# Performance work log

Measured on AMD Instinct MI355X. Metric: run time of the kernel, lower is better.

The kernel has to match this reference:

```python
import jax, jax.numpy as jnp
import numpy as np

G, N, D = 512, 400, 128   # graphs, nodes per graph, feature dim
K = 200                   # max_node_num (cluster slots per graph)
DOUT = 512
DMID = DOUT // 16         # 32


def setup_inputs() -> dict:
    key = jax.random.key(0)
    ks = jax.random.split(key, 10)
    x = jax.random.normal(ks[0], (G, N, D), dtype=jnp.float32)
    cluster = jax.random.randint(ks[1], (G, N), 0, K, dtype=jnp.int32)
    true_score = jax.random.uniform(ks[2], (G // 2, 1), dtype=jnp.float32)
    # learned parameters
    W1 = jax.random.normal(ks[3], (D, D), dtype=jnp.float32) / np.sqrt(D)
    b1 = jnp.zeros((D,), jnp.float32)
    W2 = jax.random.normal(ks[4], (DMID, K * D), dtype=jnp.float32) / np.sqrt(K * D)
    b2 = jax.random.normal(ks[5], (DMID,), dtype=jnp.float32) * 0.01
    W3 = jax.random.normal(ks[6], (DOUT, DMID), dtype=jnp.float32) / np.sqrt(DMID)
    b3 = jnp.zeros((DOUT,), jnp.float32)
    return {"x": x, "cluster": cluster, "true_score": true_score,
            "W1": W1, "b1": b1, "W2": W2, "b2": b2, "W3": W3, "b3": b3}


def reference(x, cluster, true_score, W1, b1, W2, b2, W3, b3):
    g, n, d = x.shape
    # avg_pool over clusters (scatter-mean), vectorized across all graphs
    ids = (cluster + jnp.arange(g, dtype=cluster.dtype)[:, None] * K).reshape(-1)
    flat = x.reshape(g * n, d)
    sums = jax.ops.segment_sum(flat, ids, num_segments=g * K)          # [g*K, d]
    cnt = jax.ops.segment_sum(jnp.ones((g * n,), x.dtype), ids, num_segments=g * K)
    pooled = sums / jnp.maximum(cnt, 1.0)[:, None]                     # empty clusters -> 0
    # MLP_1: Linear(D, D) + ReLU, applied per pooled node
    h = jax.nn.relu(pooled @ W1 + b1)                                  # [g*K, d]
    # flatten pooled node set; MLP_2 truncated linear == full weight on zero-padded vec
    h = h.reshape(g, K * d)
    h = jax.nn.relu(h @ W2.T + b2)                                     # [g, 32]
    # MLP_3: Linear(32, 512) + ReLU
    h = jax.nn.relu(h @ W3.T + b3)                                     # [g, 512]
    # cosine similarity between consecutive graph pairs (eps=1e-6 clamp as torch)
    g1, g2 = h[0::2], h[1::2]
    eps = 1e-6
    n1 = jnp.maximum(jnp.sqrt(jnp.sum(g1 * g1, -1)), eps)
    n2 = jnp.maximum(jnp.sqrt(jnp.sum(g2 * g2, -1)), eps)
    scores = (jnp.sum(g1 * g2, -1) / (n1 * n2))[:, None]               # [g//2, 1]
    loss = jnp.mean((scores - true_score) ** 2)                        # MSELoss
    return loss
```

## Files before the change

### kernel.cpp

```cpp
#include <hip/hip_runtime.h>
#include <math.h>

#define G 512
#define N 400
#define D 128
#define K 200
#define DOUT 512
#define DMID 32
#define GK (G*K)
#define KD (K*D)
#define NCHUNK 200

#define SH  129
#define SW2 36

#define KQ 25

__device__ __forceinline__ float relu(float v) { return fmaxf(v, 0.0f); }

typedef __attribute__((ext_vector_type(8))) short short8b;
typedef __attribute__((ext_vector_type(16))) float floatx16;

__device__ __forceinline__ ushort f2bf(float f) {
  unsigned u = __float_as_uint(f);
  unsigned r = (u + 0x7FFFu + ((u >> 16) & 1u)) >> 16;
  return (ushort)r;
}
__device__ __forceinline__ float bf2f(ushort h) {
  return __uint_as_float(((unsigned)h) << 16);
}

__global__ __launch_bounds__(256) void w1prep(
    const float* __restrict__ W1, ushort* __restrict__ wh, ushort* __restrict__ wl) {
  const int idx = blockIdx.x * 256 + threadIdx.x;
  const int i = idx & 7, l = (idx >> 3) & 63, ks = (idx >> 9) & 7, nt = idx >> 12;
  const int k = ks * 16 + (l >> 5) * 8 + i;
  const int n = nt * 32 + (l & 31);
  const float v = W1[k * D + n];
  const ushort h = f2bf(v);
  wh[idx] = h;
  wl[idx] = f2bf(v - bf2f(h));
}

__global__ __launch_bounds__(256) void pool_gemm1_fused(
    const float* __restrict__ x, const int* __restrict__ cluster,
    const ushort* __restrict__ wh, const ushort* __restrict__ wl,
    const float* __restrict__ b1, float* __restrict__ h1) {
  __shared__ int s_ids[N];
  __shared__ int s_cnt[KQ];
  __shared__ int s_off[KQ + 1];
  __shared__ int s_cur[KQ];
  __shared__ int s_sorted[N];
  __shared__ ushort sAhi[8 * 64 * 8];
  __shared__ ushort sAlo[8 * 64 * 8];
  const int g = blockIdx.y;
  const int kb = blockIdx.x * KQ;
  const int tid = threadIdx.x;
  const int* cg = cluster + g * N;

  for (int i = tid; i < N; i += 256) s_ids[i] = cg[i];
  if (tid < KQ) { s_cnt[tid] = 0; s_cur[tid] = 0; }
  {
    short8b z;
#pragma unroll
    for (int e = 0; e < 8; ++e) z[e] = 0;
    for (int i = tid; i < 512; i += 256) {
      *(short8b*)&sAhi[i * 8] = z;
      *(short8b*)&sAlo[i * 8] = z;
    }
  }
  __syncthreads();

  for (int i = tid; i < N; i += 256) {
    const int id = s_ids[i] - kb;
    if ((unsigned)id < (unsigned)KQ) atomicAdd(&s_cnt[id], 1);
  }
  __syncthreads();

  if (tid < 64) {
    const int cv = (tid < KQ) ? s_cnt[tid] : 0;
    int c = cv;
#pragma unroll
    for (int off = 1; off < 32; off <<= 1) {
      const int t = __shfl_up(c, off);
      if (tid >= off) c += t;
    }
    if (tid < KQ) s_off[tid] = c - cv;
    if (tid == KQ - 1) s_off[KQ] = c;
  }
  __syncthreads();

  for (int i = tid; i < N; i += 256) {
    const int id = s_ids[i] - kb;
    if ((unsigned)id < (unsigned)KQ) {
      const int pos = atomicAdd(&s_cur[id], 1);
      s_sorted[s_off[id] + pos] = (id << 9) | i;
    }
  }
  __syncthreads();

  const int wv = tid >> 6, l = tid & 63;
  {
    const int kl0 = (wv * KQ) >> 2;
    const int kl1 = ((wv + 1) * KQ) >> 2;
    const float* xg = x + (size_t)g * N * D + l * 2;
    const int k0 = 2 * l;
    const int ksL = k0 >> 4, kqL = (k0 >> 3) & 1, i0 = k0 & 7;

#define PL_FLUSH(KL, AX, AY, INV)                                          \
    {                                                                      \
      const int blk = ksL * 64 + ((kqL * 32 + (KL)) ^ ksL);                \
      const float fx = (AX) * (INV), fy = (AY) * (INV);                    \
      const ushort hx = f2bf(fx), hy = f2bf(fy);                           \
      ushort2 hv; hv.x = hx; hv.y = hy;                                    \
      ushort2 lv;                                                          \
      lv.x = f2bf(fx - bf2f(hx)); lv.y = f2bf(fy - bf2f(hy));              \
      *(ushort2*)&sAhi[blk * 8 + i0] = hv;                                 \
      *(ushort2*)&sAlo[blk * 8 + i0] = lv;                                 \
    }

    if (kl1 > kl0) {
      const int i0g = s_off[kl0], i1g = s_off[kl1];
      if (i1g > i0g) {
        int prev = -1;
        float ax = 0.0f, ay = 0.0f;
        int pkA[8], pkB[8];
        float2 vA[8], vB[8];

#define PL_LOAD(PK, VV, BASE)                                              \
        {                                                                  \
          _Pragma("unroll")                                                \
          for (int j = 0; j < 8; ++j) {                                    \
            const int mi = ((BASE) + j < i1g) ? (BASE) + j : i1g - 1;      \
            PK[j] = s_sorted[mi];                                          \
          }                                                                \
          _Pragma("unroll")                                                \
          for (int j = 0; j < 8; ++j)                                      \
            VV[j] = *(const float2*)&xg[(size_t)(PK[j] & 511) * D];        \
        }

#define PL_PROC(PK, VV, BASE)                                              \
        {                                                                  \
          _Pragma("unroll")                                                \
          for (int j = 0; j < 8; ++j) {                                    \
            if ((BASE) + j < i1g) {                                        \
              const int id = PK[j] >> 9;                                   \
              if (id != prev) {                                            \
                if (prev >= 0) {                                           \
                  const float inv = 1.0f / (float)s_cnt[prev];             \
                  PL_FLUSH(prev, ax, ay, inv);                             \
                }                                                          \
                ax = VV[j].x; ay = VV[j].y; prev = id;                     \
              } else { ax += VV[j].x; ay += VV[j].y; }                     \
            }                                                              \
          }                                                                \
        }

        int base = i0g;
        PL_LOAD(pkA, vA, base);
        while (base < i1g) {
          if (base + 8 < i1g) PL_LOAD(pkB, vB, base + 8);
          PL_PROC(pkA, vA, base);
          base += 8;
          if (base >= i1g) break;
          if (base + 8 < i1g) PL_LOAD(pkA, vA, base + 8);
          PL_PROC(pkB, vB, base);
          base += 8;
        }
        if (prev >= 0) {
          const float inv = 1.0f / (float)s_cnt[prev];
          PL_FLUSH(prev, ax, ay, inv);
        }
#undef PL_LOAD
#undef PL_PROC
      }
    }
#undef PL_FLUSH
  }
  __syncthreads();

  floatx16 acc0;
#pragma unroll
  for (int e = 0; e < 16; ++e) acc0[e] = 0.0f;

  const ushort* whw = wh + (size_t)(wv * 8) * 64 * 8;
  const ushort* wlw = wl + (size_t)(wv * 8) * 64 * 8;

#pragma unroll 2
  for (int ks = 0; ks < 8; ++ks) {
    const int lx = l ^ ks;
    const short8b bh = *(const short8b*)&whw[(ks * 64 + l) * 8];
    const short8b bl = *(const short8b*)&wlw[(ks * 64 + l) * 8];
    const short8b ah = *(const short8b*)&sAhi[(ks * 64 + lx) * 8];
    const short8b al = *(const short8b*)&sAlo[(ks * 64 + lx) * 8];
    acc0 = __builtin_amdgcn_mfma_f32_32x32x16_bf16(ah, bh, acc0, 0, 0, 0);
    acc0 = __builtin_amdgcn_mfma_f32_32x32x16_bf16(ah, bl, acc0, 0, 0, 0);
    acc0 = __builtin_amdgcn_mfma_f32_32x32x16_bf16(al, bh, acc0, 0, 0, 0);
  }

  const int col = l & 31;
  const int n = wv * 32 + col;
  const float bias = b1[n];
  const int rbase = 4 * (l >> 5);
  float* hrow = h1 + ((size_t)g * K + kb) * D + n;
#pragma unroll
  for (int e = 0; e < 16; ++e) {
    const int row = (e & 3) + 8 * (e >> 2) + rbase;
    if (row < KQ) hrow[(size_t)row * D] = relu(acc0[e] + bias);
  }
}

__global__ __launch_bounds__(256) void gemm2_partial(
    const float* __restrict__ h1, const float* __restrict__ W2,
    float* __restrict__ partials) {
  extern __shared__ float smem[];
  float* sHt = smem;
  float* sWT = smem + 32 * SH;
  const int kc = blockIdx.x;
  const int gb = blockIdx.y;
  const int k0 = kc * 128, g0 = gb * 32;
  const int tid = threadIdx.x;

  for (int i = tid; i < 32 * 128; i += 256) {
    const int r = i >> 7, k = i & 127;
    sHt[r * SH + k] = h1[(size_t)(g0 + r) * KD + k0 + k];
  }
  for (int i = tid; i < 32 * 128; i += 256) {
    const int j = i >> 7, k = i & 127;
    sWT[k * SW2 + j] = W2[(size_t)j * KD + k0 + k];
  }
  __syncthreads();

  const int jt = tid & 7;
  const int gt = tid >> 3;
  float acc[4];
#pragma unroll
  for (int j = 0; j < 4; j++) acc[j] = 0.0f;

  for (int k = 0; k < 128; ++k) {
    const float h = sHt[gt * SH + k];
    const float4 w0 = *(const float4*)&sWT[k * SW2 + jt * 4];
    acc[0] = fmaf(h, w0.x, acc[0]); acc[1] = fmaf(h, w0.y, acc[1]);
    acc[2] = fmaf(h, w0.z, acc[2]); acc[3] = fmaf(h, w0.w, acc[3]);
  }

  float* pp = partials + ((size_t)kc * G + g0 + gt) * DMID + jt * 4;
  *(float4*)&pp[0] = make_float4(acc[0], acc[1], acc[2], acc[3]);
}

__global__ __launch_bounds__(256) void gemm2_reduce(
    const float* __restrict__ partials, const float* __restrict__ b2,
    float* __restrict__ h2) {
  __shared__ float s_red[3][64];
  const int tid = threadIdx.x;
  const int li = tid & 63;
  const int w = tid >> 6;
  const int idx = blockIdx.x * 64 + li;
  float s = 0.0f;
#pragma unroll 5
  for (int c = w * 50; c < w * 50 + 50; ++c)
    s += partials[(size_t)c * (G * DMID) + idx];
  if (w > 0) s_red[w - 1][li] = s;
  __syncthreads();
  if (w == 0) {
    s += s_red[0][li] + s_red[1][li] + s_red[2][li];
    h2[idx] = relu(s + b2[idx & 31]);
  }
}

__global__ __launch_bounds__(256) void head_kernel(
    const float* __restrict__ h2, const float* __restrict__ W3,
    const float* __restrict__ b3, const float* __restrict__ ts,
    float* __restrict__ pair_sq) {
  __shared__ float sA[DMID], sB[DMID];
  __shared__ float rdot[4], rna[4], rnb[4];
  const int p = blockIdx.x;
  const int tid = threadIdx.x;
  if (tid < DMID) sA[tid] = h2[(size_t)(2 * p) * DMID + tid];
  else if (tid < 2 * DMID) sB[tid - DMID] = h2[(size_t)(2 * p + 1) * DMID + (tid - DMID)];
  __syncthreads();

  float dot = 0.0f, na = 0.0f, nb = 0.0f;
#pragma unroll
  for (int rep = 0; rep < 2; ++rep) {
    const int o = rep * 256 + tid;
    const float* w = W3 + (size_t)o * DMID;
    float accA = b3[o], accB = accA;
#pragma unroll
    for (int m = 0; m < DMID; m += 4) {
      const float4 wv = *(const float4*)&w[m];
      accA = fmaf(sA[m], wv.x, accA); accB = fmaf(sB[m], wv.x, accB);
      accA = fmaf(sA[m + 1], wv.y, accA); accB = fmaf(sB[m + 1], wv.y, accB);
      accA = fmaf(sA[m + 2], wv.z, accA); accB = fmaf(sB[m + 2], wv.z, accB);
      accA = fmaf(sA[m + 3], wv.w, accA); accB = fmaf(sB[m + 3], wv.w, accB);
    }
    const float a = relu(accA), b = relu(accB);
    dot = fmaf(a, b, dot); na = fmaf(a, a, na); nb = fmaf(b, b, nb);
  }
#pragma unroll
  for (int off = 32; off >= 1; off >>= 1) {
    dot += __shfl_down(dot, off);
    na  += __shfl_down(na, off);
    nb  += __shfl_down(nb, off);
  }
  const int wave = tid >> 6, lane = tid & 63;
  if (lane == 0) { rdot[wave] = dot; rna[wave] = na; rnb[wave] = nb; }
  __syncthreads();
  if (tid == 0) {
    const float dt = rdot[0] + rdot[1] + rdot[2] + rdot[3];
    const float nA = rna[0] + rna[1] + rna[2] + rna[3];
    const float nB = rnb[0] + rnb[1] + rnb[2] + rnb[3];
    const float n1 = fmaxf(sqrtf(nA), 1e-6f);
    const float n2 = fmaxf(sqrtf(nB), 1e-6f);
    const float sc = dt / (n1 * n2);
    const float e = sc - ts[p];
    pair_sq[p] = e * e;
  }
}

__global__ __launch_bounds__(256) void loss_kernel(
    const float* __restrict__ pair_sq, float* __restrict__ out) {
  __shared__ float red[4];
  const int tid = threadIdx.x;
  float v = pair_sq[tid];
#pragma unroll
  for (int off = 32; off >= 1; off >>= 1) v += __shfl_down(v, off);
  const int wave = tid >> 6, lane = tid & 63;
  if (lane == 0) red[wave] = v;
  __syncthreads();
  if (tid == 0) out[0] = (red[0] + red[1] + red[2] + red[3]) * (1.0f / 256.0f);
}

extern "C" void kernel_launch(void* const* d_in, const int* in_sizes, int n_in,
                              void* d_out, int out_size, void* d_ws, size_t ws_size,
                              hipStream_t stream) {
  const float* x       = (const float*)d_in[0];
  const int*   cluster = (const int*)d_in[1];
  const float* ts      = (const float*)d_in[2];
  const float* W1      = (const float*)d_in[3];
  const float* b1      = (const float*)d_in[4];
  const float* W2      = (const float*)d_in[5];
  const float* b2      = (const float*)d_in[6];
  const float* W3      = (const float*)d_in[7];
  const float* b3      = (const float*)d_in[8];

  float* ws = (float*)d_ws;
  float* h1        = ws;
  float* partials  = h1 + (size_t)GK * D;
  float* h2        = partials + (size_t)NCHUNK * G * DMID;
  float* pair_sq   = h2 + (size_t)G * DMID;
  ushort* wfrag_hi = (ushort*)(pair_sq + 256);
  ushort* wfrag_lo = wfrag_hi + 16384;

  w1prep<<<16384 / 256, 256, 0, stream>>>(W1, wfrag_hi, wfrag_lo);
  dim3 gridP(8, G);
  pool_gemm1_fused<<<gridP, 256, 0, stream>>>(x, cluster, wfrag_hi, wfrag_lo, b1, h1);
  dim3 gridC(NCHUNK, 16);
  gemm2_partial<<<gridC, 256, (32 * SH + 128 * SW2) * sizeof(float), stream>>>(h1, W2, partials);
  gemm2_reduce<<<G * DMID / 64, 256, 0, stream>>>(partials, b2, h2);
  head_kernel<<<G / 2, 256, 0, stream>>>(h2, W3, b3, ts, pair_sq);
  loss_kernel<<<1, 256, 0, stream>>>(pair_sq, (float*)d_out);
}
```

Baseline: 89.76 us.

## Replace GEMM2 partial buffer and loss reduction kernels with global float atomics

GEMM2 split-K partials are now accumulated directly into a zeroed h2 buffer with global float atomic adds, which removes the partials buffer and the separate reduce kernel. The MSE loss is likewise accumulated with an atomic add from the head kernel, so the final loss kernel is gone. Zeroing of the accumulators is folded into an extra block of the W1 prep launch. This cuts two launches and the partials round trip through memory. In exchange, 200-way atomic contention lands on each h2 element, and the summation order becomes nondeterministic.

New measurement: 142.2 us. 1.58x slower.

```diff
diff --git a/kernel.cpp b/kernel.cpp
--- a/kernel.cpp
+++ b/kernel.cpp
@@ -9,7 +9,6 @@
 #define DMID 32
 #define GK (G*K)
 #define KD (K*D)
-#define NCHUNK 200
 
 #define SH  129
 #define SW2 36
@@ -30,8 +29,21 @@
   return __uint_as_float(((unsigned)h) << 16);
 }
 
+__device__ __forceinline__ void gl_fadd(float* p, float v) {
+  asm volatile("global_atomic_add_f32 %0, %1, off"
+               :
+               : "v"(p), "v"(v)
+               : "memory");
+}
+
 __global__ __launch_bounds__(256) void w1prep(
-    const float* __restrict__ W1, ushort* __restrict__ wh, ushort* __restrict__ wl) {
+    const float* __restrict__ W1, ushort* __restrict__ wh, ushort* __restrict__ wl,
+    float* __restrict__ h2pre, float* __restrict__ out) {
+  if (blockIdx.x == 64) {
+    for (int i = threadIdx.x; i < G * DMID; i += 256) h2pre[i] = 0.0f;
+    if (threadIdx.x == 0) out[0] = 0.0f;
+    return;
+  }
   const int idx = blockIdx.x * 256 + threadIdx.x;
   const int i = idx & 7, l = (idx >> 3) & 63, ks = (idx >> 9) & 7, nt = idx >> 12;
   const int k = ks * 16 + (l >> 5) * 8 + i;
@@ -212,7 +224,7 @@
 
 __global__ __launch_bounds__(256) void gemm2_partial(
     const float* __restrict__ h1, const float* __restrict__ W2,
-    float* __restrict__ partials) {
+    float* __restrict__ h2pre) {
   extern __shared__ float smem[];
   float* sHt = smem;
   float* sWT = smem + 32 * SH;
@@ -244,40 +256,25 @@
     acc[2] = fmaf(h, w0.z, acc[2]); acc[3] = fmaf(h, w0.w, acc[3]);
   }
 
-  float* pp = partials + ((size_t)kc * G + g0 + gt) * DMID + jt * 4;
-  *(float4*)&pp[0] = make_float4(acc[0], acc[1], acc[2], acc[3]);
-}
-
-__global__ __launch_bounds__(256) void gemm2_reduce(
-    const float* __restrict__ partials, const float* __restrict__ b2,
-    float* __restrict__ h2) {
-  __shared__ float s_red[3][64];
-  const int tid = threadIdx.x;
-  const int li = tid & 63;
-  const int w = tid >> 6;
-  const int idx = blockIdx.x * 64 + li;
-  float s = 0.0f;
-#pragma unroll 5
-  for (int c = w * 50; c < w * 50 + 50; ++c)
-    s += partials[(size_t)c * (G * DMID) + idx];
-  if (w > 0) s_red[w - 1][li] = s;
-  __syncthreads();
-  if (w == 0) {
-    s += s_red[0][li] + s_red[1][li] + s_red[2][li];
-    h2[idx] = relu(s + b2[idx & 31]);
-  }
+  float* pp = h2pre + (size_t)(g0 + gt) * DMID + jt * 4;
+  gl_fadd(&pp[0], acc[0]);
+  gl_fadd(&pp[1], acc[1]);
+  gl_fadd(&pp[2], acc[2]);
+  gl_fadd(&pp[3], acc[3]);
 }
 
 __global__ __launch_bounds__(256) void head_kernel(
-    const float* __restrict__ h2, const float* __restrict__ W3,
-    const float* __restrict__ b3, const float* __restrict__ ts,
-    float* __restrict__ pair_sq) {
+    const float* __restrict__ h2pre, const float* __restrict__ b2,
+    const float* __restrict__ W3, const float* __restrict__ b3,
+    const float* __restrict__ ts, float* __restrict__ out) {
   __shared__ float sA[DMID], sB[DMID];
   __shared__ float rdot[4], rna[4], rnb[4];
   const int p = blockIdx.x;
   const int tid = threadIdx.x;
-  if (tid < DMID) sA[tid] = h2[(size_t)(2 * p) * DMID + tid];
-  else if (tid < 2 * DMID) sB[tid - DMID] = h2[(size_t)(2 * p + 1) * DMID + (tid - DMID)];
+  if (tid < DMID)
+    sA[tid] = relu(h2pre[(size_t)(2 * p) * DMID + tid] + b2[tid]);
+  else if (tid < 2 * DMID)
+    sB[tid - DMID] = relu(h2pre[(size_t)(2 * p + 1) * DMID + (tid - DMID)] + b2[tid - DMID]);
   __syncthreads();
 
   float dot = 0.0f, na = 0.0f, nb = 0.0f;
@@ -314,21 +311,8 @@
     const float n2 = fmaxf(sqrtf(nB), 1e-6f);
     const float sc = dt / (n1 * n2);
     const float e = sc - ts[p];
-    pair_sq[p] = e * e;
-  }
-}
-
-__global__ __launch_bounds__(256) void loss_kernel(
-    const float* __restrict__ pair_sq, float* __restrict__ out) {
-  __shared__ float red[4];
-  const int tid = threadIdx.x;
-  float v = pair_sq[tid];
-#pragma unroll
-  for (int off = 32; off >= 1; off >>= 1) v += __shfl_down(v, off);
-  const int wave = tid >> 6, lane = tid & 63;
-  if (lane == 0) red[wave] = v;
-  __syncthreads();
-  if (tid == 0) out[0] = (red[0] + red[1] + red[2] + red[3]) * (1.0f / 256.0f);
+    gl_fadd(out, e * e * (1.0f / 256.0f));
+  }
 }
 
 extern "C" void kernel_launch(void* const* d_in, const int* in_sizes, int n_in,
@@ -346,18 +330,15 @@
 
   float* ws = (float*)d_ws;
   float* h1        = ws;
-  float* partials  = h1 + (size_t)GK * D;
-  float* h2        = partials + (size_t)NCHUNK * G * DMID;
-  float* pair_sq   = h2 + (size_t)G * DMID;
-  ushort* wfrag_hi = (ushort*)(pair_sq + 256);
+  float* h2pre     = h1 + (size_t)GK * D;
+  ushort* wfrag_hi = (ushort*)(h2pre + (size_t)G * DMID);
   ushort* wfrag_lo = wfrag_hi + 16384;
-
-  w1prep<<<16384 / 256, 256, 0, stream>>>(W1, wfrag_hi, wfrag_lo);
+  float* out       = (float*)d_out;
+
+  w1prep<<<65, 256, 0, stream>>>(W1, wfrag_hi, wfrag_lo, h2pre, out);
   dim3 gridP(8, G);
   pool_gemm1_fused<<<gridP, 256, 0, stream>>>(x, cluster, wfrag_hi, wfrag_lo, b1, h1);
-  dim3 gridC(NCHUNK, 16);
-  gemm2_partial<<<gridC, 256, (32 * SH + 128 * SW2) * sizeof(float), stream>>>(h1, W2, partials);
-  gemm2_reduce<<<G * DMID / 64, 256, 0, stream>>>(partials, b2, h2);
-  head_kernel<<<G / 2, 256, 0, stream>>>(h2, W3, b3, ts, pair_sq);
-  loss_kernel<<<1, 256, 0, stream>>>(pair_sq, (float*)d_out);
-}
+  dim3 gridC(200, 16);
+  gemm2_partial<<<gridC, 256, (32 * SH + 128 * SW2) * sizeof(float), stream>>>(h1, W2, h2pre);
+  head_kernel<<<G / 2, 256, 0, stream>>>(h2pre, b2, W3, b3, ts, out);
+}
```
